# Kernel tuning notes

Hardware: AMD Instinct MI355X
Metric: run time of the kernel (lower is better)

Reference implementation:

```python
import jax, jax.numpy as jnp
import numpy as np

K = 5  # top-k neighbors (init kwarg k)
EPS = 1e-12

def _normalize(x):
    n = jnp.linalg.norm(x, axis=1, keepdims=True)
    return x / jnp.maximum(n, EPS)

def setup_inputs() -> dict:
    key = jax.random.key(0)
    k1, k2, k3 = jax.random.split(key, 3)
    B, D, N, C = 1024, 1024, 100000, 1000
    features = jax.random.normal(k1, (B, D), dtype=jnp.float32)
    idx = jax.random.randint(k2, (B,), 0, N, dtype=jnp.int64)
    # buffers: feat_memory = F.normalize(rand(N, D)); pred_memory = ones(N, C)/C
    feat_memory = _normalize(jax.random.uniform(k3, (N, D), dtype=jnp.float32))
    pred_memory = jnp.ones((N, C), dtype=jnp.float32) / C
    return {"features": features, "idx": idx,
            "feat_memory": feat_memory, "pred_memory": pred_memory}

def reference(features, idx, feat_memory, pred_memory):
    B = features.shape[0]
    x = _normalize(features)                       # [B, D]
    dis = x @ feat_memory.T                        # [B, N] similarity
    # self-mask: each row's own bank entry set to global min (min is invariant
    # under this assignment, so the per-row torch loop vectorizes exactly)
    m = jnp.min(dis)
    dis = dis.at[jnp.arange(B), idx].set(m)
    _, indices = jax.lax.top_k(dis, K)             # [B, K]
    mean_logits = jnp.mean(pred_memory[indices], axis=1)  # [B, C]
    pseudo_labels = jnp.argmax(mean_logits, axis=1)       # [B]
    return pseudo_labels, mean_logits
```

## Files before the change

kernel.cpp:

```cpp
#include <hip/hip_runtime.h>
#include <stdint.h>
#include <stddef.h>

#define B_ROWS 1024
#define D_DIM  1024
#define N_MEM  100000
#define C_CLS  1000
#define K_TOP  5

#define TM 128
#define TN 128
#define BK 32
#define NT_TILES ((N_MEM + TN - 1) / TN)
#define BT_TILES (B_ROWS / TM)
#define NPAD (NT_TILES * TN)

typedef __bf16 bf16;
typedef bf16 bf16x4 __attribute__((ext_vector_type(4)));
typedef bf16 bf16x8 __attribute__((ext_vector_type(8)));
typedef float f32x4 __attribute__((ext_vector_type(4)));

__global__ __launch_bounds__(256) void k_normalize(const float* __restrict__ F,
                                                   bf16* __restrict__ X) {
  int row = blockIdx.x;
  int tid = threadIdx.x;
  const float4* fr = (const float4*)(F + (size_t)row * D_DIM);
  float4 v = fr[tid];
  float s = v.x * v.x + v.y * v.y + v.z * v.z + v.w * v.w;
  for (int off = 32; off > 0; off >>= 1) s += __shfl_down(s, off, 64);
  __shared__ float wred[4];
  if ((tid & 63) == 0) wred[tid >> 6] = s;
  __syncthreads();
  float tot = wred[0] + wred[1] + wred[2] + wred[3];
  float inv = 1.0f / fmaxf(sqrtf(tot), 1e-12f);
  bf16x4 o;
  o[0] = (bf16)(v.x * inv);
  o[1] = (bf16)(v.y * inv);
  o[2] = (bf16)(v.z * inv);
  o[3] = (bf16)(v.w * inv);
  *(bf16x4*)(X + (size_t)row * D_DIM + (size_t)tid * 4) = o;
}

__global__ __launch_bounds__(256) void k_convert(const float* __restrict__ FM,
                                                 bf16* __restrict__ FMB, int total4) {
  int i = blockIdx.x * 256 + threadIdx.x;
  if (i >= total4) return;
  float4 v = ((const float4*)FM)[i];
  bf16x4 o;
  o[0] = (bf16)v.x; o[1] = (bf16)v.y; o[2] = (bf16)v.z; o[3] = (bf16)v.w;
  ((bf16x4*)FMB)[i] = o;
}

__device__ __forceinline__ void gl_lds16(const bf16* g, bf16* l) {
  __builtin_amdgcn_global_load_lds((__attribute__((address_space(1))) void*)g,
                                   (__attribute__((address_space(3))) void*)l,
                                   16, 0, 0);
}

__global__ __launch_bounds__(256) void k_gemm(const bf16* __restrict__ X,
                                              const bf16* __restrict__ FMB,
                                              bf16* __restrict__ DIS) {
  __shared__ bf16 As[TM * BK];
  __shared__ bf16 Bs[TN * BK];
  int bt = blockIdx.x & (BT_TILES - 1);
  int nt = blockIdx.x >> 3;
  size_t row0 = (size_t)bt * TM;
  size_t col0 = (size_t)nt * TN;
  int tid = threadIdx.x;
  int lane = tid & 63;
  int wv = tid >> 6;
  int wm = wv >> 1, wn = wv & 1;

  f32x4 acc[4][4];
  for (int mi = 0; mi < 4; ++mi)
    for (int ni = 0; ni < 4; ++ni)
      acc[mi][ni] = (f32x4){0.f, 0.f, 0.f, 0.f};

  int frow = lane & 15;
  int kq = (lane >> 4) * 8;

  const bf16* Xbase = X + row0 * D_DIM;
  const bf16* Fbase = FMB + col0 * D_DIM;

  for (int k0 = 0; k0 < D_DIM; k0 += BK) {
    __syncthreads();
    for (int r = 0; r < 2; ++r) {
      int c = r * 256 + tid;
      int arow = c >> 2;
      int ac = (c & 3) * 8;
      gl_lds16(Xbase + (size_t)arow * D_DIM + k0 + ac, As + (size_t)c * 8);
      gl_lds16(Fbase + (size_t)arow * D_DIM + k0 + ac, Bs + (size_t)c * 8);
    }
    __syncthreads();

    bf16x8 af[4], bfr[4];
    for (int mi = 0; mi < 4; ++mi)
      af[mi] = *(const bf16x8*)&As[(size_t)(wm * 64 + mi * 16 + frow) * BK + kq];
    for (int ni = 0; ni < 4; ++ni)
      bfr[ni] = *(const bf16x8*)&Bs[(size_t)(wn * 64 + ni * 16 + frow) * BK + kq];
    for (int mi = 0; mi < 4; ++mi)
      for (int ni = 0; ni < 4; ++ni)
        acc[mi][ni] = __builtin_amdgcn_mfma_f32_16x16x32_bf16(af[mi], bfr[ni],
                                                              acc[mi][ni], 0, 0, 0);
  }

  int orow = (lane >> 4) * 4;
  int ocol = lane & 15;
  for (int mi = 0; mi < 4; ++mi)
    for (int ni = 0; ni < 4; ++ni)
      for (int r = 0; r < 4; ++r) {
        size_t gr = row0 + (size_t)(wm * 64 + mi * 16 + orow + r);
        size_t gc = col0 + (size_t)(wn * 64 + ni * 16 + ocol);
        DIS[gr * NPAD + gc] = (bf16)acc[mi][ni][r];
      }
}

__device__ void gather_mean_argmax(const int* find, const float* __restrict__ P,
                                   float* __restrict__ OUT, int b, int tid) {
  float bestV = -1e30f;
  int bestC = 0;
  for (int c = tid; c < C_CLS; c += 256) {
    float s = 0.f;
    for (int j = 0; j < K_TOP; ++j) s += P[(size_t)find[j] * C_CLS + c];
    float mean = s * (1.0f / K_TOP);
    OUT[(size_t)B_ROWS + (size_t)b * C_CLS + c] = mean;
    if (mean > bestV) { bestV = mean; bestC = c; }
  }
  __shared__ float rv[256];
  __shared__ int rc[256];
  rv[tid] = bestV; rc[tid] = bestC;
  for (int s = 128; s >= 1; s >>= 1) {
    __syncthreads();
    if (tid < s) {
      float v2 = rv[tid + s]; int c2 = rc[tid + s];
      if (v2 > rv[tid] || (v2 == rv[tid] && c2 < rc[tid])) { rv[tid] = v2; rc[tid] = c2; }
    }
  }
  __syncthreads();
  if (tid == 0) OUT[b] = (float)rc[0];
}

__global__ __launch_bounds__(256) void k_topk(const bf16* __restrict__ DIS,
                                              const int* __restrict__ IDX,
                                              const float* __restrict__ P,
                                              float* __restrict__ OUT) {
  int b = blockIdx.x;
  int tid = threadIdx.x;
  int self = IDX[b];
  const bf16* drow = DIS + (size_t)b * NPAD;

  float tv[K_TOP]; int ti[K_TOP];
  for (int j = 0; j < K_TOP; ++j) { tv[j] = -1e30f; ti[j] = 0; }
  for (int n = tid; n < N_MEM; n += 256) {
    if (n == self) continue;
    float v = (float)drow[n];
    if (v > tv[K_TOP - 1]) {
      int p = K_TOP - 1;
      while (p > 0 && v > tv[p - 1]) { tv[p] = tv[p - 1]; ti[p] = ti[p - 1]; --p; }
      tv[p] = v; ti[p] = n;
    }
  }
  __shared__ float sv[256 * K_TOP];
  __shared__ int si[256 * K_TOP];
  for (int j = 0; j < K_TOP; ++j) { sv[tid * K_TOP + j] = tv[j]; si[tid * K_TOP + j] = ti[j]; }
  for (int s = 128; s >= 1; s >>= 1) {
    __syncthreads();
    if (tid < s) {
      float av[K_TOP], bv[K_TOP]; int ai[K_TOP], bi[K_TOP];
      for (int j = 0; j < K_TOP; ++j) {
        av[j] = sv[tid * K_TOP + j];       ai[j] = si[tid * K_TOP + j];
        bv[j] = sv[(tid + s) * K_TOP + j]; bi[j] = si[(tid + s) * K_TOP + j];
      }
      float ov[K_TOP]; int oi[K_TOP];
      int i2 = 0, j2 = 0;
      for (int t = 0; t < K_TOP; ++t) {
        if (j2 >= K_TOP || (i2 < K_TOP && av[i2] >= bv[j2])) { ov[t] = av[i2]; oi[t] = ai[i2]; ++i2; }
        else { ov[t] = bv[j2]; oi[t] = bi[j2]; ++j2; }
      }
      for (int j = 0; j < K_TOP; ++j) { sv[tid * K_TOP + j] = ov[j]; si[tid * K_TOP + j] = oi[j]; }
    }
  }
  __syncthreads();
  __shared__ int find[K_TOP];
  if (tid < K_TOP) {
    int v = si[tid];
    find[tid] = (v < 0) ? 0 : (v >= N_MEM ? N_MEM - 1 : v);
  }
  __syncthreads();
  gather_mean_argmax(find, P, OUT, b, tid);
}

__global__ __launch_bounds__(256) void k_naive(const float* __restrict__ F,
                                               const int* __restrict__ IDX,
                                               const float* __restrict__ FM,
                                               const float* __restrict__ P,
                                               float* __restrict__ OUT) {
  int b = blockIdx.x;
  int tid = threadIdx.x;
  __shared__ float xs[D_DIM];
  __shared__ float wred[4];
  const float4* fr = (const float4*)(F + (size_t)b * D_DIM);
  float4 v = fr[tid];
  float s = v.x * v.x + v.y * v.y + v.z * v.z + v.w * v.w;
  for (int off = 32; off > 0; off >>= 1) s += __shfl_down(s, off, 64);
  if ((tid & 63) == 0) wred[tid >> 6] = s;
  __syncthreads();
  float inv = 1.0f / fmaxf(sqrtf(wred[0] + wred[1] + wred[2] + wred[3]), 1e-12f);
  float4 xv = make_float4(v.x * inv, v.y * inv, v.z * inv, v.w * inv);
  ((float4*)xs)[tid] = xv;
  __syncthreads();
  int self = IDX[b];
  __shared__ float ptv[K_TOP];
  __shared__ int pti[K_TOP];
  if (tid < K_TOP) { ptv[tid] = -1e30f; pti[tid] = 0; }
  __syncthreads();
  for (int n = 0; n < N_MEM; ++n) {
    const float4* frow = (const float4*)(FM + (size_t)n * D_DIM);
    float4 fv = frow[tid];
    float p = xv.x * fv.x + xv.y * fv.y + xv.z * fv.z + xv.w * fv.w;
    for (int off = 32; off > 0; off >>= 1) p += __shfl_down(p, off, 64);
    if ((tid & 63) == 0) wred[tid >> 6] = p;
    __syncthreads();
    if (tid == 0 && n != self) {
      float tot = wred[0] + wred[1] + wred[2] + wred[3];
      if (tot > ptv[K_TOP - 1]) {
        int q = K_TOP - 1;
        while (q > 0 && tot > ptv[q - 1]) { ptv[q] = ptv[q - 1]; pti[q] = pti[q - 1]; --q; }
        ptv[q] = tot; pti[q] = n;
      }
    }
    __syncthreads();
  }
  __shared__ int find[K_TOP];
  if (tid < K_TOP) {
    int x = pti[tid];
    find[tid] = (x < 0) ? 0 : (x >= N_MEM ? N_MEM - 1 : x);
  }
  __syncthreads();
  gather_mean_argmax(find, P, OUT, b, tid);
}

extern "C" void kernel_launch(void* const* d_in, const int* in_sizes, int n_in,
                              void* d_out, int out_size, void* d_ws, size_t ws_size,
                              hipStream_t stream) {
  const float* F  = (const float*)d_in[0];
  const int* IDX  = (const int*)d_in[1];
  const float* FM = (const float*)d_in[2];
  const float* P  = (const float*)d_in[3];
  float* OUT = (float*)d_out;

  const size_t xBytes  = (size_t)B_ROWS * D_DIM * 2;
  const size_t fmBytes = (size_t)NPAD * D_DIM * 2;
  const size_t disBytes = (size_t)B_ROWS * NPAD * 2;
  const size_t need = xBytes + fmBytes + disBytes;

  if (ws_size >= need) {
    bf16* X   = (bf16*)d_ws;
    bf16* FMB = (bf16*)((char*)d_ws + xBytes);
    bf16* DIS = (bf16*)((char*)d_ws + xBytes + fmBytes);
    k_normalize<<<B_ROWS, 256, 0, stream>>>(F, X);
    int total4 = N_MEM * D_DIM / 4;
    k_convert<<<(total4 + 255) / 256, 256, 0, stream>>>(FM, FMB, total4);
    k_gemm<<<NT_TILES * BT_TILES, 256, 0, stream>>>(X, FMB, DIS);
    k_topk<<<B_ROWS, 256, 0, stream>>>(DIS, IDX, P, OUT);
  } else {
    k_naive<<<B_ROWS, 256, 0, stream>>>(F, IDX, FM, P, OUT);
  }
}
```

Measured before the change: 1.260 ms.

## Fuse per-tile top-5 selection into GEMM epilogue and add XCD-aware tiling

The GEMM now writes its 128x128 similarity tile to shared memory and computes a per-row top-5 for each tile there, emitting only candidates instead of the full bf16 B×N similarity matrix. A separate merge kernel reduces the per-tile candidates and does the gather/mean/argmax. The LDS layout for A/B is XOR-swizzled to cut bank conflicts, and block indices are remapped so each XCD handles a contiguous range of N tiles, which improves L2 reuse of the feature bank. This removes a large global write and read of the distance matrix, at the cost of extra LDS use and a serial epilogue in each GEMM block.

```diff
diff --git a/kernel.cpp b/kernel.cpp
--- a/kernel.cpp
+++ b/kernel.cpp
@@ -14,11 +14,23 @@
 #define NT_TILES ((N_MEM + TN - 1) / TN)
 #define BT_TILES (B_ROWS / TM)
 #define NPAD (NT_TILES * TN)
+#define NTL_PER_XCD ((NT_TILES + 7) / 8)
+#define SS_LD (TN + 4)
 
 typedef __bf16 bf16;
 typedef bf16 bf16x4 __attribute__((ext_vector_type(4)));
 typedef bf16 bf16x8 __attribute__((ext_vector_type(8)));
 typedef float f32x4 __attribute__((ext_vector_type(4)));
+
+__device__ __forceinline__ void insert5(float v, int n, float tv[K_TOP], int ti[K_TOP]) {
+#pragma unroll
+  for (int j = 0; j < K_TOP; ++j) {
+    bool gt = v > tv[j];
+    float ov = tv[j]; int oi = ti[j];
+    tv[j] = gt ? v : ov;  ti[j] = gt ? n : oi;
+    v = gt ? ov : v;      n = gt ? oi : n;
+  }
+}
 
 __global__ __launch_bounds__(256) void k_normalize(const float* __restrict__ F,
                                                    bf16* __restrict__ X) {
@@ -57,13 +69,23 @@
                                    16, 0, 0);
 }
 
-__global__ __launch_bounds__(256) void k_gemm(const bf16* __restrict__ X,
-                                              const bf16* __restrict__ FMB,
-                                              bf16* __restrict__ DIS) {
-  __shared__ bf16 As[TM * BK];
-  __shared__ bf16 Bs[TN * BK];
-  int bt = blockIdx.x & (BT_TILES - 1);
-  int nt = blockIdx.x >> 3;
+__global__ __launch_bounds__(256) void k_gemm_topk(const bf16* __restrict__ X,
+                                                   const bf16* __restrict__ FMB,
+                                                   const int* __restrict__ IDX,
+                                                   float2* __restrict__ CAND) {
+  __shared__ __align__(16) char shm[2 * TM * BK * 2];
+  __shared__ bf16 Ss[TM * SS_LD];
+  bf16* As = (bf16*)shm;
+  bf16* Bs = As + TM * BK;
+
+  int bid = blockIdx.x;
+  int xcd = bid & 7;
+  int rest = bid >> 3;
+  int bt = rest & 7;
+  int ntl = rest >> 3;
+  int nt = xcd * NTL_PER_XCD + ntl;
+  if (nt >= NT_TILES) return;
+
   size_t row0 = (size_t)bt * TM;
   size_t col0 = (size_t)nt * TN;
   int tid = threadIdx.x;
@@ -77,7 +99,7 @@
       acc[mi][ni] = (f32x4){0.f, 0.f, 0.f, 0.f};
 
   int frow = lane & 15;
-  int kq = (lane >> 4) * 8;
+  int q = lane >> 4;
 
   const bf16* Xbase = X + row0 * D_DIM;
   const bf16* Fbase = FMB + col0 * D_DIM;
@@ -87,17 +109,23 @@
     for (int r = 0; r < 2; ++r) {
       int c = r * 256 + tid;
       int arow = c >> 2;
-      int ac = (c & 3) * 8;
-      gl_lds16(Xbase + (size_t)arow * D_DIM + k0 + ac, As + (size_t)c * 8);
-      gl_lds16(Fbase + (size_t)arow * D_DIM + k0 + ac, Bs + (size_t)c * 8);
+      int j = (c & 3) ^ ((arow >> 1) & 3);
+      gl_lds16(Xbase + (size_t)arow * D_DIM + k0 + j * 8, As + (size_t)c * 8);
+      gl_lds16(Fbase + (size_t)arow * D_DIM + k0 + j * 8, Bs + (size_t)c * 8);
     }
     __syncthreads();
 
     bf16x8 af[4], bfr[4];
-    for (int mi = 0; mi < 4; ++mi)
-      af[mi] = *(const bf16x8*)&As[(size_t)(wm * 64 + mi * 16 + frow) * BK + kq];
-    for (int ni = 0; ni < 4; ++ni)
-      bfr[ni] = *(const bf16x8*)&Bs[(size_t)(wn * 64 + ni * 16 + frow) * BK + kq];
+    for (int mi = 0; mi < 4; ++mi) {
+      int r = wm * 64 + mi * 16 + frow;
+      int slot = r * 4 + (q ^ ((r >> 1) & 3));
+      af[mi] = *(const bf16x8*)&As[(size_t)slot * 8];
+    }
+    for (int ni = 0; ni < 4; ++ni) {
+      int r = wn * 64 + ni * 16 + frow;
+      int slot = r * 4 + (q ^ ((r >> 1) & 3));
+      bfr[ni] = *(const bf16x8*)&Bs[(size_t)slot * 8];
+    }
     for (int mi = 0; mi < 4; ++mi)
       for (int ni = 0; ni < 4; ++ni)
         acc[mi][ni] = __builtin_amdgcn_mfma_f32_16x16x32_bf16(af[mi], bfr[ni],
@@ -108,11 +136,38 @@
   int ocol = lane & 15;
   for (int mi = 0; mi < 4; ++mi)
     for (int ni = 0; ni < 4; ++ni)
-      for (int r = 0; r < 4; ++r) {
-        size_t gr = row0 + (size_t)(wm * 64 + mi * 16 + orow + r);
-        size_t gc = col0 + (size_t)(wn * 64 + ni * 16 + ocol);
-        DIS[gr * NPAD + gc] = (bf16)acc[mi][ni][r];
-      }
+      for (int r = 0; r < 4; ++r)
+        Ss[(size_t)(wm * 64 + mi * 16 + orow + r) * SS_LD + (wn * 64 + ni * 16 + ocol)]
+            = (bf16)acc[mi][ni][r];
+  __syncthreads();
+
+  int tr = tid >> 1, h = tid & 1;
+  int grow = (int)row0 + tr;
+  int self = IDX[grow];
+  float tv[K_TOP]; int ti[K_TOP];
+  for (int j = 0; j < K_TOP; ++j) { tv[j] = -1e30f; ti[j] = -1; }
+  for (int c = 0; c < 64; ++c) {
+    int cc = h * 64 + c;
+    int gc = (int)col0 + cc;
+    if (gc >= N_MEM || gc == self) continue;
+    float v = (float)Ss[(size_t)tr * SS_LD + cc];
+    if (v > tv[K_TOP - 1]) insert5(v, gc, tv, ti);
+  }
+
+  float* mv = (float*)shm;
+  int* mi_ = (int*)(shm + 8192);
+  for (int j = 0; j < K_TOP; ++j) { mv[tid * K_TOP + j] = tv[j]; mi_[tid * K_TOP + j] = ti[j]; }
+  __syncthreads();
+  if (h == 0) {
+    for (int j = 0; j < K_TOP; ++j) {
+      float v = mv[(tid + 1) * K_TOP + j];
+      int n = mi_[(tid + 1) * K_TOP + j];
+      if (v > tv[K_TOP - 1]) insert5(v, n, tv, ti);
+    }
+    float2* out = CAND + ((size_t)grow * NT_TILES + nt) * K_TOP;
+    for (int j = 0; j < K_TOP; ++j)
+      out[j] = make_float2(tv[j], __int_as_float(ti[j]));
+  }
 }
 
 __device__ void gather_mean_argmax(const int* find, const float* __restrict__ P,
@@ -140,52 +195,42 @@
   if (tid == 0) OUT[b] = (float)rc[0];
 }
 
-__global__ __launch_bounds__(256) void k_topk(const bf16* __restrict__ DIS,
-                                              const int* __restrict__ IDX,
-                                              const float* __restrict__ P,
-                                              float* __restrict__ OUT) {
+__global__ __launch_bounds__(256) void k_merge(const float2* __restrict__ CAND,
+                                               const float* __restrict__ P,
+                                               float* __restrict__ OUT) {
   int b = blockIdx.x;
   int tid = threadIdx.x;
-  int self = IDX[b];
-  const bf16* drow = DIS + (size_t)b * NPAD;
+  const float2* row = CAND + (size_t)b * (NT_TILES * K_TOP);
 
   float tv[K_TOP]; int ti[K_TOP];
-  for (int j = 0; j < K_TOP; ++j) { tv[j] = -1e30f; ti[j] = 0; }
-  for (int n = tid; n < N_MEM; n += 256) {
-    if (n == self) continue;
-    float v = (float)drow[n];
-    if (v > tv[K_TOP - 1]) {
-      int p = K_TOP - 1;
-      while (p > 0 && v > tv[p - 1]) { tv[p] = tv[p - 1]; ti[p] = ti[p - 1]; --p; }
-      tv[p] = v; ti[p] = n;
-    }
-  }
+  for (int j = 0; j < K_TOP; ++j) { tv[j] = -1e30f; ti[j] = -1; }
+  for (int i = tid; i < NT_TILES * K_TOP; i += 256) {
+    float2 e = row[i];
+    float v = e.x;
+    if (v > tv[K_TOP - 1]) insert5(v, __float_as_int(e.y), tv, ti);
+  }
+
   __shared__ float sv[256 * K_TOP];
   __shared__ int si[256 * K_TOP];
   for (int j = 0; j < K_TOP; ++j) { sv[tid * K_TOP + j] = tv[j]; si[tid * K_TOP + j] = ti[j]; }
   for (int s = 128; s >= 1; s >>= 1) {
     __syncthreads();
     if (tid < s) {
-      float av[K_TOP], bv[K_TOP]; int ai[K_TOP], bi[K_TOP];
       for (int j = 0; j < K_TOP; ++j) {
-        av[j] = sv[tid * K_TOP + j];       ai[j] = si[tid * K_TOP + j];
-        bv[j] = sv[(tid + s) * K_TOP + j]; bi[j] = si[(tid + s) * K_TOP + j];
+        float v = sv[(tid + s) * K_TOP + j];
+        int n = si[(tid + s) * K_TOP + j];
+        if (v > tv[K_TOP - 1]) insert5(v, n, tv, ti);
       }
-      float ov[K_TOP]; int oi[K_TOP];
-      int i2 = 0, j2 = 0;
-      for (int t = 0; t < K_TOP; ++t) {
-        if (j2 >= K_TOP || (i2 < K_TOP && av[i2] >= bv[j2])) { ov[t] = av[i2]; oi[t] = ai[i2]; ++i2; }
-        else { ov[t] = bv[j2]; oi[t] = bi[j2]; ++j2; }
-      }
-      for (int j = 0; j < K_TOP; ++j) { sv[tid * K_TOP + j] = ov[j]; si[tid * K_TOP + j] = oi[j]; }
+      for (int j = 0; j < K_TOP; ++j) { sv[tid * K_TOP + j] = tv[j]; si[tid * K_TOP + j] = ti[j]; }
     }
   }
   __syncthreads();
   __shared__ int find[K_TOP];
-  if (tid < K_TOP) {
-    int v = si[tid];
-    find[tid] = (v < 0) ? 0 : (v >= N_MEM ? N_MEM - 1 : v);
-  }
+  if (tid == 0)
+    for (int j = 0; j < K_TOP; ++j) {
+      int v = si[j];
+      find[j] = (v < 0) ? 0 : (v >= N_MEM ? N_MEM - 1 : v);
+    }
   __syncthreads();
   gather_mean_argmax(find, P, OUT, b, tid);
 }
@@ -197,7 +242,6 @@
                                                float* __restrict__ OUT) {
   int b = blockIdx.x;
   int tid = threadIdx.x;
-  __shared__ float xs[D_DIM];
   __shared__ float wred[4];
   const float4* fr = (const float4*)(F + (size_t)b * D_DIM);
   float4 v = fr[tid];
@@ -207,7 +251,6 @@
   __syncthreads();
   float inv = 1.0f / fmaxf(sqrtf(wred[0] + wred[1] + wred[2] + wred[3]), 1e-12f);
   float4 xv = make_float4(v.x * inv, v.y * inv, v.z * inv, v.w * inv);
-  ((float4*)xs)[tid] = xv;
   __syncthreads();
   int self = IDX[b];
   __shared__ float ptv[K_TOP];
@@ -249,20 +292,20 @@
   const float* P  = (const float*)d_in[3];
   float* OUT = (float*)d_out;
 
-  const size_t xBytes  = (size_t)B_ROWS * D_DIM * 2;
-  const size_t fmBytes = (size_t)NPAD * D_DIM * 2;
-  const size_t disBytes = (size_t)B_ROWS * NPAD * 2;
-  const size_t need = xBytes + fmBytes + disBytes;
+  const size_t xBytes    = (size_t)B_ROWS * D_DIM * 2;
+  const size_t fmBytes   = (size_t)NPAD * D_DIM * 2;
+  const size_t candBytes = (size_t)B_ROWS * NT_TILES * K_TOP * 8;
+  const size_t need = xBytes + fmBytes + candBytes;
 
   if (ws_size >= need) {
-    bf16* X   = (bf16*)d_ws;
-    bf16* FMB = (bf16*)((char*)d_ws + xBytes);
-    bf16* DIS = (bf16*)((char*)d_ws + xBytes + fmBytes);
+    bf16* X      = (bf16*)d_ws;
+    bf16* FMB    = (bf16*)((char*)d_ws + xBytes);
+    float2* CAND = (float2*)((char*)d_ws + xBytes + fmBytes);
     k_normalize<<<B_ROWS, 256, 0, stream>>>(F, X);
     int total4 = N_MEM * D_DIM / 4;
     k_convert<<<(total4 + 255) / 256, 256, 0, stream>>>(FM, FMB, total4);
-    k_gemm<<<NT_TILES * BT_TILES, 256, 0, stream>>>(X, FMB, DIS);
-    k_topk<<<B_ROWS, 256, 0, stream>>>(DIS, IDX, P, OUT);
+    k_gemm_topk<<<8 * NTL_PER_XCD * BT_TILES, 256, 0, stream>>>(X, FMB, IDX, CAND);
+    k_merge<<<B_ROWS, 256, 0, stream>>>(CAND, P, OUT);
   } else {
     k_naive<<<B_ROWS, 256, 0, stream>>>(F, IDX, FM, P, OUT);
   }
```

New measurement: 1.071 ms. -15.0%, faster.
